# Optimization experiments

Measured on AMD Instinct MI355X. Metric: run time of the kernel, lower is better.

Reference implementation:

```python
import jax, jax.numpy as jnp
import numpy as np

D_MODEL = 1024
B, T = 4, 2048
LN_EPS = 1e-5


def setup_inputs() -> dict:
    key = jax.random.key(0)
    ks = jax.random.split(key, 8)
    d = D_MODEL
    x = jax.random.normal(ks[0], (B, T, d), dtype=jnp.float32)
    # linear params (fan-in scaled)
    W_in = jax.random.normal(ks[1], (d, 4 * d), dtype=jnp.float32) / np.sqrt(d)
    b_in = jnp.zeros((4 * d,), dtype=jnp.float32)
    W_out = jax.random.normal(ks[2], (2 * d, d), dtype=jnp.float32) / np.sqrt(2 * d)
    b_out = jnp.zeros((d,), dtype=jnp.float32)
    # LRU initializer (matches the torch module's initializer())
    rng = np.random.default_rng(0)
    r_min, r_max = 0.9, 0.999
    u1 = rng.random(d)
    u2 = rng.random(d)
    nu_log = np.log(-0.5 * np.log(u1 * (r_max ** 2 - r_min ** 2) + r_min ** 2))
    theta_log = np.log(u2 * np.pi * 2)
    gamma_log = np.log(np.sqrt(1 - np.exp(-np.exp(nu_log)) ** 2))
    # LayerNorm affine params
    ln_w = jnp.ones((2 * d,), dtype=jnp.float32)
    ln_b = jnp.zeros((2 * d,), dtype=jnp.float32)
    return {
        "x": x,
        "W_in": W_in, "b_in": b_in,
        "nu_log": jnp.asarray(nu_log, dtype=jnp.float32),
        "theta_log": jnp.asarray(theta_log, dtype=jnp.float32),
        "gamma_log": jnp.asarray(gamma_log, dtype=jnp.float32),
        "ln_w": ln_w, "ln_b": ln_b,
        "W_out": W_out, "b_out": b_out,
    }


def _complex_scan(in_r, in_i, f_r, f_i):
    """h_t = f * h_{t-1} + in_t over axis=1, complex math in real/imag pairs."""
    def combine(l, r):
        a1r, a1i, b1r, b1i = l
        a2r, a2i, b2r, b2i = r
        ar = a2r * a1r - a2i * a1i
        ai = a2r * a1i + a2i * a1r
        br = a2r * b1r - a2i * b1i + b2r
        bi = a2r * b1i + a2i * b1r + b2i
        return (ar, ai, br, bi)
    fr = jnp.broadcast_to(f_r, in_r.shape)
    fi = jnp.broadcast_to(f_i, in_i.shape)
    _, _, hr, hi = jax.lax.associative_scan(combine, (fr, fi, in_r, in_i), axis=1)
    return hr, hi


def reference(x, W_in, b_in, nu_log, theta_log, gamma_log, ln_w, ln_b, W_out, b_out):
    d = x.shape[-1]
    u = x @ W_in + b_in                       # [B, T, 4d]
    v, o = u[..., :2 * d], u[..., 2 * d:]     # each [B, T, 2d]
    nu = jnp.exp(-jnp.exp(nu_log))            # [d]
    theta = jnp.exp(theta_log)
    gamma = jnpp_exp = jnp.exp(gamma_log)
    f_r = nu * jnp.cos(theta)
    f_i = nu * jnp.sin(theta)
    in_r = gamma * v[..., :d]                 # [B, T, d]
    in_i = gamma * v[..., d:]
    h_r, h_i = _complex_scan(in_r, in_i, f_r, f_i)
    y = jnp.concatenate([h_r, h_i], axis=-1) * jax.nn.silu(o)  # [B, T, 2d]
    mu = jnp.mean(y, axis=-1, keepdims=True)
    var = jnp.mean(jnp.square(y - mu), axis=-1, keepdims=True)
    y = (y - mu) * jax.lax.rsqrt(var + LN_EPS) * ln_w + ln_b
    return y @ W_out + b_out                  # [B, T, d]
```

## Files before the change

kernel.cpp:

```cpp
#include <hip/hip_runtime.h>
#include <hip/hip_bf16.h>

#define D_MODEL 1024
#define BB 4
#define TT 2048
#define ROWS (BB*TT)
#define NCHUNK 64
#define CHLEN 32

typedef __attribute__((ext_vector_type(8))) short short8;
typedef __attribute__((ext_vector_type(4))) float floatx4;

static __device__ __forceinline__ ushort f2bf(float f) {
    union { float f; unsigned u; } v; v.f = f;
    unsigned r = v.u + 0x7FFF + ((v.u >> 16) & 1);
    return (ushort)(r >> 16);
}
static __device__ __forceinline__ float bf2f(ushort b) {
    union { unsigned u; float f; } v; v.u = ((unsigned)b) << 16;
    return v.f;
}

#define GLOAD_LDS16(gp, lp)                                                 \
    __builtin_amdgcn_global_load_lds(                                       \
        (const __attribute__((address_space(1))) void*)(gp),                \
        (__attribute__((address_space(3))) void*)(lp), 16, 0, 0)

#define PREP_A 8192
#define PREP_B 4096
#define PREP_C 2048
__global__ __launch_bounds__(256) void prep_all(
    const float* __restrict__ x, ushort* __restrict__ xb,
    const float* __restrict__ W_in, ushort* __restrict__ WinT,
    const float* __restrict__ W_out, ushort* __restrict__ W1T,
    const float* __restrict__ lnw, const float* __restrict__ lnb,
    float* __restrict__ s1, float* __restrict__ c2,
    const float* __restrict__ nu_log, const float* __restrict__ theta_log,
    const float* __restrict__ gamma_log,
    float* __restrict__ fr, float* __restrict__ fi, float* __restrict__ gm) {
    __shared__ float smem[32 * 33 + 8 * 32 * 2];
    int bid = blockIdx.x, tid = threadIdx.x;
    if (bid < PREP_A) {
        int i = bid * 256 + tid;
        float4 v = ((const float4*)x)[i];
        ushort4 o;
        o.x = f2bf(v.x); o.y = f2bf(v.y); o.z = f2bf(v.z); o.w = f2bf(v.w);
        ((ushort4*)xb)[i] = o;
    } else if (bid < PREP_A + PREP_B) {
        int b2 = bid - PREP_A;
        int n0 = (b2 & 127) * 32, k0 = (b2 >> 7) * 32;
        int tx = tid & 31, ty = tid >> 5;
        float (*tile)[33] = (float (*)[33])smem;
#pragma unroll
        for (int j = 0; j < 4; ++j)
            tile[ty + j*8][tx] = W_in[(size_t)(k0 + ty + j*8) * 4096 + n0 + tx];
        __syncthreads();
#pragma unroll
        for (int j = 0; j < 4; ++j)
            WinT[(size_t)(n0 + ty + j*8) * 1024 + k0 + tx] = f2bf(tile[tx][ty + j*8]);
    } else if (bid < PREP_A + PREP_B + PREP_C) {
        int b2 = bid - PREP_A - PREP_B;
        int n0 = (b2 & 31) * 32, k0 = (b2 >> 5) * 32;
        int tx = tid & 31, ty = tid >> 5;
        float (*tile)[33] = (float (*)[33])smem;
        float* red1 = smem + 32 * 33;
        float* red2 = red1 + 8 * 32;
        float p1 = 0.f, p2 = 0.f;
#pragma unroll
        for (int j = 0; j < 4; ++j) {
            int k = k0 + ty + j * 8;
            float w = W_out[(size_t)k * 1024 + n0 + tx];
            float lw = lnw[k], lb = lnb[k];
            tile[ty + j*8][tx] = lw * w;
            p1 += lw * w; p2 += lb * w;
        }
        __syncthreads();
#pragma unroll
        for (int j = 0; j < 4; ++j)
            W1T[(size_t)(n0 + ty + j*8) * 2048 + k0 + tx] = f2bf(tile[tx][ty + j*8]);
        red1[ty * 32 + tx] = p1; red2[ty * 32 + tx] = p2;
        __syncthreads();
        if (ty == 0) {
            float a = 0.f, b = 0.f;
#pragma unroll
            for (int t = 0; t < 8; ++t) { a += red1[t * 32 + tx]; b += red2[t * 32 + tx]; }
            atomicAdd(&s1[n0 + tx], a);
            atomicAdd(&c2[n0 + tx], b);
        }
    } else {
        int c = (bid - PREP_A - PREP_B - PREP_C) * 256 + tid;
        if (c < D_MODEL) {
            float nu = expf(-expf(nu_log[c]));
            float th = expf(theta_log[c]);
            fr[c] = nu * cosf(th);
            fi[c] = nu * sinf(th);
            gm[c] = expf(gamma_log[c]);
        }
    }
}

#define P_PRE  do { __builtin_amdgcn_sched_barrier(0); __builtin_amdgcn_s_barrier();  \
                    asm volatile("s_waitcnt lgkmcnt(0)" ::: "memory");                \
                    __builtin_amdgcn_sched_barrier(0);                                \
                    __builtin_amdgcn_s_setprio(1); } while (0)
#define P_POST do { __builtin_amdgcn_s_setprio(0); __builtin_amdgcn_sched_barrier(0); \
                    __builtin_amdgcn_s_barrier();                                     \
                    __builtin_amdgcn_sched_barrier(0); } while (0)

__global__ __launch_bounds__(512) void gemm256(
    const ushort* __restrict__ A, const ushort* __restrict__ B,
    int K, const float* __restrict__ bias,
    const float* __restrict__ gamma,
    ushort* __restrict__ out_r, ushort* __restrict__ out_i,
    ushort* __restrict__ out_o) {
    __shared__ ushort LA[2][256 * 64];
    __shared__ ushort LB[2][256 * 64];
    int tid = threadIdx.x;
    int lane = tid & 63;
    int wave = tid >> 6;
    int wp = wave >> 2;
    int wq = wave & 3;
    int lr = lane & 15, q = lane >> 4;
    int swl = lr & 7;
    int rs8 = tid >> 3, ch = tid & 7;
    int sw8 = (ch ^ (rs8 & 7)) * 8;

    int gx = gridDim.x;
    int nwg = gx * gridDim.y;
    int lid = blockIdx.y * gx + blockIdx.x;
    int per = nwg >> 3;
    int sid = (lid & 7) * per + (lid >> 3);
    long m0 = (long)(sid / gx) * 256;
    long n0 = (long)(sid % gx) * 256;
    const int NT = K >> 6;

    const ushort* Abase = A + (size_t)(m0 + rs8) * K + sw8;
    const ushort* Bbase = B + (size_t)(n0 + rs8) * K + sw8;

    floatx4 acc[8][4] = {};

#define STG_A(kt, P, R) GLOAD_LDS16(Abase + (size_t)(R) * K + (kt), \
                                    &LA[P][((R) + rs8) * 64 + ch * 8])
#define STG_B(kt, P, R) GLOAD_LDS16(Bbase + (size_t)(R) * K + (kt), \
                                    &LB[P][((R) + rs8) * 64 + ch * 8])

    STG_A(0, 0, 0);    STG_A(0, 0, 64);
    STG_B(0, 0, 0);    STG_B(0, 0, 64);
    STG_B(0, 0, 128);  STG_B(0, 0, 192);
    STG_A(0, 0, 128);  STG_A(0, 0, 192);
    STG_A(64, 1, 0);   STG_A(64, 1, 64);
    STG_B(64, 1, 0);   STG_B(64, 1, 64);
    STG_B(64, 1, 128); STG_B(64, 1, 192);
    asm volatile("s_waitcnt vmcnt(6)" ::: "memory");
    __builtin_amdgcn_s_barrier();

    for (int t = 0; t < NT; ++t) {
        const int p = t & 1;
        int kt1 = (t + 1 < NT) ? (t + 1) << 6 : 0;
        int kt2 = (t + 2 < NT) ? (t + 2) << 6 : 0;
        short8 a[2][4], b0[2][2], b1[2][2];

#pragma unroll
        for (int ks = 0; ks < 2; ++ks) {
#pragma unroll
            for (int r = 0; r < 4; ++r)
                a[ks][r] = *(const short8*)&LA[p][(wp * 64 + r * 16 + lr) * 64 + ((ks * 4 + q) ^ swl) * 8];
#pragma unroll
            for (int c = 0; c < 2; ++c)
                b0[ks][c] = *(const short8*)&LB[p][(wq * 32 + c * 16 + lr) * 64 + ((ks * 4 + q) ^ swl) * 8];
        }
        STG_A(kt1, p ^ 1, 128); STG_A(kt1, p ^ 1, 192);
        P_PRE;
#pragma unroll
        for (int ks = 0; ks < 2; ++ks)
#pragma unroll
            for (int r = 0; r < 4; ++r)
#pragma unroll
                for (int c = 0; c < 2; ++c)
                    acc[r][c] = __builtin_amdgcn_mfma_f32_16x16x32_bf16(
                        a[ks][r], b0[ks][c], acc[r][c], 0, 0, 0);
        P_POST;

#pragma unroll
        for (int ks = 0; ks < 2; ++ks)
#pragma unroll
            for (int c = 0; c < 2; ++c)
                b1[ks][c] = *(const short8*)&LB[p][(128 + wq * 32 + c * 16 + lr) * 64 + ((ks * 4 + q) ^ swl) * 8];
        STG_A(kt2, p, 0); STG_A(kt2, p, 64);
        P_PRE;
#pragma unroll
        for (int ks = 0; ks < 2; ++ks)
#pragma unroll
            for (int r = 0; r < 4; ++r)
#pragma unroll
                for (int c = 0; c < 2; ++c)
                    acc[r][2 + c] = __builtin_amdgcn_mfma_f32_16x16x32_bf16(
                        a[ks][r], b1[ks][c], acc[r][2 + c], 0, 0, 0);
        P_POST;

#pragma unroll
        for (int ks = 0; ks < 2; ++ks)
#pragma unroll
            for (int r = 0; r < 4; ++r)
                a[ks][r] = *(const short8*)&LA[p][(128 + wp * 64 + r * 16 + lr) * 64 + ((ks * 4 + q) ^ swl) * 8];
        STG_B(kt2, p, 0); STG_B(kt2, p, 64);
        P_PRE;
#pragma unroll
        for (int ks = 0; ks < 2; ++ks)
#pragma unroll
            for (int r = 0; r < 4; ++r)
#pragma unroll
                for (int c = 0; c < 2; ++c)
                    acc[4 + r][c] = __builtin_amdgcn_mfma_f32_16x16x32_bf16(
                        a[ks][r], b0[ks][c], acc[4 + r][c], 0, 0, 0);
        P_POST;

        STG_B(kt2, p, 128); STG_B(kt2, p, 192);
        asm volatile("s_waitcnt vmcnt(6)" ::: "memory");
        P_PRE;
#pragma unroll
        for (int ks = 0; ks < 2; ++ks)
#pragma unroll
            for (int r = 0; r < 4; ++r)
#pragma unroll
                for (int c = 0; c < 2; ++c)
                    acc[4 + r][2 + c] = __builtin_amdgcn_mfma_f32_16x16x32_bf16(
                        a[ks][r], b1[ks][c], acc[4 + r][2 + c], 0, 0, 0);
        P_POST;
    }
    asm volatile("s_waitcnt vmcnt(0)" ::: "memory");

    int sector = (int)(n0 >> 10);
    if (sector < 2) {
        ushort* dst = sector ? out_i : out_r;
#pragma unroll
        for (int nh = 0; nh < 2; ++nh)
#pragma unroll
            for (int c = 0; c < 2; ++c) {
                int lc = (int)(n0 & 1023) + nh * 128 + wq * 32 + c * 16 + lr;
                float bv = bias[(sector << 10) + lc];
                float gv = gamma[lc];
#pragma unroll
                for (int mh = 0; mh < 2; ++mh)
#pragma unroll
                    for (int r = 0; r < 4; ++r)
#pragma unroll
                        for (int g = 0; g < 4; ++g) {
                            long row = m0 + mh * 128 + wp * 64 + r * 16 + q * 4 + g;
                            dst[row * 1024 + lc] = f2bf(gv * (acc[mh * 4 + r][nh * 2 + c][g] + bv));
                        }
            }
    } else {
        int oc0 = (int)(n0 - 2048);
#pragma unroll
        for (int nh = 0; nh < 2; ++nh)
#pragma unroll
            for (int c = 0; c < 2; ++c) {
                int oc = oc0 + nh * 128 + wq * 32 + c * 16 + lr;
                float bv = bias[2048 + oc];
#pragma unroll
                for (int mh = 0; mh < 2; ++mh)
#pragma unroll
                    for (int r = 0; r < 4; ++r)
#pragma unroll
                        for (int g = 0; g < 4; ++g) {
                            long row = m0 + mh * 128 + wp * 64 + r * 16 + q * 4 + g;
                            out_o[row * 2048 + oc] = f2bf(acc[mh * 4 + r][nh * 2 + c][g] + bv);
                        }
            }
    }
#undef STG_A
#undef STG_B
}

__global__ __launch_bounds__(512) void gemm2_2t(
    const ushort* __restrict__ A, const ushort* __restrict__ B,
    int K, int N, const float* __restrict__ bias, float* __restrict__ outC,
    const float* __restrict__ mu, const float* __restrict__ rs,
    const float* __restrict__ s1, const float* __restrict__ c2) {
    __shared__ ushort LA[2][128 * 64];
    __shared__ ushort LB[2][256 * 64];
    int tid = threadIdx.x;
    int lane = tid & 63;
    int wave = tid >> 6;
    int wp = wave >> 2;
    int wq = wave & 3;
    int lr = lane & 15, q = lane >> 4;
    int swl = lr & 7;
    int rs8 = tid >> 3, ch = tid & 7;
    int sw8 = (ch ^ (rs8 & 7)) * 8;

    int gx = gridDim.x;
    int nwg = gx * gridDim.y;
    int lid = blockIdx.y * gx + blockIdx.x;
    int per = nwg >> 3;
    int sid = (lid & 7) * per + (lid >> 3);
    long m0 = (long)(sid / gx) * 128;
    long n0 = (long)(sid % gx) * 256;
    const int NT = K >> 6;
    const int NI = NT >> 1;

    const ushort* Abase = A + (size_t)(m0 + rs8) * K + sw8;
    const ushort* Bbase = B + (size_t)(n0 + rs8) * K + sw8;

    floatx4 acc[4][4] = {};

#define STG2_A(kt, P, R) GLOAD_LDS16(Abase + (size_t)(R) * K + (kt), \
                                     &LA[P][((R) + rs8) * 64 + ch * 8])
#define STG2_B(kt, P, R) GLOAD_LDS16(Bbase + (size_t)(R) * K + (kt), \
                                     &LB[P][((R) + rs8) * 64 + ch * 8])
#define STG2_TILE(kt, P) do { STG2_A(kt, P, 0); STG2_A(kt, P, 64);            \
                              STG2_B(kt, P, 0); STG2_B(kt, P, 64);            \
                              STG2_B(kt, P, 128); STG2_B(kt, P, 192); } while (0)

    STG2_TILE(0, 0);
    asm volatile("s_waitcnt vmcnt(0)" ::: "memory");
    __builtin_amdgcn_s_barrier();

    for (int i = 0; i < NI; ++i) {
        int t0 = 2 * i;
        int kt1 = (t0 + 1) << 6;
        int kt2 = (t0 + 2 < NT) ? (t0 + 2) << 6 : 0;
        short8 a[2][2], b0[2][2], b1[2][2];

#pragma unroll
        for (int ks = 0; ks < 2; ++ks) {
#pragma unroll
            for (int r = 0; r < 2; ++r)
                a[ks][r] = *(const short8*)&LA[0][(wp * 32 + r * 16 + lr) * 64 + ((ks * 4 + q) ^ swl) * 8];
#pragma unroll
            for (int c = 0; c < 2; ++c) {
                b0[ks][c] = *(const short8*)&LB[0][(wq * 32 + c * 16 + lr) * 64 + ((ks * 4 + q) ^ swl) * 8];
                b1[ks][c] = *(const short8*)&LB[0][(128 + wq * 32 + c * 16 + lr) * 64 + ((ks * 4 + q) ^ swl) * 8];
            }
        }
        STG2_TILE(kt1, 1);
        P_PRE;
#pragma unroll
        for (int ks = 0; ks < 2; ++ks)
#pragma unroll
            for (int r = 0; r < 2; ++r)
#pragma unroll
                for (int c = 0; c < 2; ++c) {
                    acc[r][c] = __builtin_amdgcn_mfma_f32_16x16x32_bf16(
                        a[ks][r], b0[ks][c], acc[r][c], 0, 0, 0);
                    acc[r][2 + c] = __builtin_amdgcn_mfma_f32_16x16x32_bf16(
                        a[ks][r], b1[ks][c], acc[r][2 + c], 0, 0, 0);
                }
        P_POST;

#pragma unroll
        for (int ks = 0; ks < 2; ++ks)
#pragma unroll
            for (int r = 0; r < 2; ++r)
                a[ks][r] = *(const short8*)&LA[0][(64 + wp * 32 + r * 16 + lr) * 64 + ((ks * 4 + q) ^ swl) * 8];
        P_PRE;
#pragma unroll
        for (int ks = 0; ks < 2; ++ks)
#pragma unroll
            for (int r = 0; r < 2; ++r)
#pragma unroll
                for (int c = 0; c < 2; ++c) {
                    acc[2 + r][c] = __builtin_amdgcn_mfma_f32_16x16x32_bf16(
                        a[ks][r], b0[ks][c], acc[2 + r][c], 0, 0, 0);
                    acc[2 + r][2 + c] = __builtin_amdgcn_mfma_f32_16x16x32_bf16(
                        a[ks][r], b1[ks][c], acc[2 + r][2 + c], 0, 0, 0);
                }
        asm volatile("s_waitcnt vmcnt(0)" ::: "memory");
        P_POST;

#pragma unroll
        for (int ks = 0; ks < 2; ++ks) {
#pragma unroll
            for (int r = 0; r < 2; ++r)
                a[ks][r] = *(const short8*)&LA[1][(wp * 32 + r * 16 + lr) * 64 + ((ks * 4 + q) ^ swl) * 8];
#pragma unroll
            for (int c = 0; c < 2; ++c) {
                b0[ks][c] = *(const short8*)&LB[1][(wq * 32 + c * 16 + lr) * 64 + ((ks * 4 + q) ^ swl) * 8];
                b1[ks][c] = *(const short8*)&LB[1][(128 + wq * 32 + c * 16 + lr) * 64 + ((ks * 4 + q) ^ swl) * 8];
            }
        }
        STG2_TILE(kt2, 0);
        P_PRE;
#pragma unroll
        for (int ks = 0; ks < 2; ++ks)
#pragma unroll
            for (int r = 0; r < 2; ++r)
#pragma unroll
                for (int c = 0; c < 2; ++c) {
                    acc[r][c] = __builtin_amdgcn_mfma_f32_16x16x32_bf16(
                        a[ks][r], b0[ks][c], acc[r][c], 0, 0, 0);
                    acc[r][2 + c] = __builtin_amdgcn_mfma_f32_16x16x32_bf16(
                        a[ks][r], b1[ks][c], acc[r][2 + c], 0, 0, 0);
                }
        P_POST;

#pragma unroll
        for (int ks = 0; ks < 2; ++ks)
#pragma unroll
            for (int r = 0; r < 2; ++r)
                a[ks][r] = *(const short8*)&LA[1][(64 + wp * 32 + r * 16 + lr) * 64 + ((ks * 4 + q) ^ swl) * 8];
        P_PRE;
#pragma unroll
        for (int ks = 0; ks < 2; ++ks)
#pragma unroll
            for (int r = 0; r < 2; ++r)
#pragma unroll
                for (int c = 0; c < 2; ++c) {
                    acc[2 + r][c] = __builtin_amdgcn_mfma_f32_16x16x32_bf16(
                        a[ks][r], b0[ks][c], acc[2 + r][c], 0, 0, 0);
                    acc[2 + r][2 + c] = __builtin_amdgcn_mfma_f32_16x16x32_bf16(
                        a[ks][r], b1[ks][c], acc[2 + r][2 + c], 0, 0, 0);
                }
        asm volatile("s_waitcnt vmcnt(0)" ::: "memory");
        P_POST;
    }
    asm volatile("s_waitcnt vmcnt(0)" ::: "memory");

#pragma unroll
    for (int nh = 0; nh < 2; ++nh)
#pragma unroll
        for (int c = 0; c < 2; ++c) {
            long col = n0 + nh * 128 + wq * 32 + c * 16 + lr;
            float bc = c2[col] + bias[col];
            float s1c = s1[col];
#pragma unroll
            for (int mh = 0; mh < 2; ++mh)
#pragma unroll
                for (int r = 0; r < 2; ++r)
#pragma unroll
                    for (int g = 0; g < 4; ++g) {
                        long row = m0 + mh * 64 + wp * 32 + r * 16 + q * 4 + g;
                        outC[row * (long)N + col] =
                            rs[row] * (acc[mh * 2 + r][nh * 2 + c][g] - mu[row] * s1c) + bc;
                    }
        }
#undef STG2_A
#undef STG2_B
#undef STG2_TILE
}

__global__ __launch_bounds__(256) void scan_carries(
    const ushort* __restrict__ in_r, const ushort* __restrict__ in_i,
    float* __restrict__ carry,
    const float* __restrict__ fr_, const float* __restrict__ fi_) {
    int t = blockIdx.x * 256 + threadIdx.x;
    int cp = t & 511;
    int ck = (t >> 9) & (NCHUNK - 1);
    int b = t >> 15;
    int c0 = cp * 2;
    float f0r = fr_[c0], f0i = fi_[c0], f1r = fr_[c0 + 1], f1i = fi_[c0 + 1];
    size_t base = ((size_t)(b * TT + ck * CHLEN)) * 1024 + c0;
    float h0r = 0.f, h0i = 0.f, h1r = 0.f, h1i = 0.f;
#pragma unroll 8
    for (int j = 0; j < CHLEN; ++j) {
        uint ur = *(const uint*)(in_r + base + (size_t)j * 1024);
        uint ui = *(const uint*)(in_i + base + (size_t)j * 1024);
        float r0 = bf2f((ushort)ur), r1 = bf2f((ushort)(ur >> 16));
        float i0 = bf2f((ushort)ui), i1 = bf2f((ushort)(ui >> 16));
        float n0r = f0r * h0r - f0i * h0i + r0;
        float n0i = f0r * h0i + f0i * h0r + i0;
        float n1r = f1r * h1r - f1i * h1i + r1;
        float n1i = f1r * h1i + f1i * h1r + i1;
        h0r = n0r; h0i = n0i; h1r = n1r; h1i = n1i;
    }
    ((float4*)carry)[((size_t)b * NCHUNK + ck) * 512 + cp] =
        make_float4(h0r, h0i, h1r, h1i);
}

__global__ __launch_bounds__(256) void carry_prefix(
    float* __restrict__ carry,
    const float* __restrict__ fr_, const float* __restrict__ fi_) {
    int t = blockIdx.x * 256 + threadIdx.x;
    int cp = t & 511, b = t >> 9;
    int c0 = cp * 2;
    float a0r = fr_[c0], a0i = fi_[c0], a1r = fr_[c0 + 1], a1i = fi_[c0 + 1];
#pragma unroll
    for (int s = 0; s < 5; ++s) {
        float t0r = a0r * a0r - a0i * a0i, t0i = 2.f * a0r * a0i;
        float t1r = a1r * a1r - a1i * a1i, t1i = 2.f * a1r * a1i;
        a0r = t0r; a0i = t0i; a1r = t1r; a1i = t1i;
    }
    float4* base = (float4*)carry + (size_t)b * NCHUNK * 512 + cp;
    float C0r = 0.f, C0i = 0.f, C1r = 0.f, C1i = 0.f;
    for (int k = 0; k < NCHUNK; ++k) {
        float4 s = base[(size_t)k * 512];
        base[(size_t)k * 512] = make_float4(C0r, C0i, C1r, C1i);
        float n0r = a0r * C0r - a0i * C0i + s.x;
        float n0i = a0r * C0i + a0i * C0r + s.y;
        float n1r = a1r * C1r - a1i * C1i + s.z;
        float n1i = a1r * C1i + a1i * C1r + s.w;
        C0r = n0r; C0i = n0i; C1r = n1r; C1i = n1i;
    }
}

__global__ __launch_bounds__(256) void scan_apply(
    const ushort* __restrict__ in_r, const ushort* __restrict__ in_i,
    const float* __restrict__ carry,
    const float* __restrict__ fr_, const float* __restrict__ fi_,
    const ushort* __restrict__ o, ushort* __restrict__ yb) {
    int t = blockIdx.x * 256 + threadIdx.x;
    int cp = t & 511;
    int ck = (t >> 9) & (NCHUNK - 1);
    int b = t >> 15;
    int c0 = cp * 2;
    float f0r = fr_[c0], f0i = fi_[c0], f1r = fr_[c0 + 1], f1i = fi_[c0 + 1];
    float4 C = ((const float4*)carry)[((size_t)b * NCHUNK + ck) * 512 + cp];
    float h0r = C.x, h0i = C.y, h1r = C.z, h1i = C.w;
    size_t base = ((size_t)(b * TT + ck * CHLEN)) * 1024 + c0;
    size_t rowbase = (size_t)(b * TT + ck * CHLEN);
#pragma unroll 4
    for (int j = 0; j < CHLEN; ++j) {
        uint ur = *(const uint*)(in_r + base + (size_t)j * 1024);
        uint ui = *(const uint*)(in_i + base + (size_t)j * 1024);
        size_t ob = (rowbase + j) * 2048 + c0;
        uint uo1 = *(const uint*)(o + ob);
        uint uo2 = *(const uint*)(o + ob + 1024);
        float r0 = bf2f((ushort)ur), r1 = bf2f((ushort)(ur >> 16));
        float i0 = bf2f((ushort)ui), i1 = bf2f((ushort)(ui >> 16));
        float n0r = f0r * h0r - f0i * h0i + r0;
        float n0i = f0r * h0i + f0i * h0r + i0;
        float n1r = f1r * h1r - f1i * h1i + r1;
        float n1i = f1r * h1i + f1i * h1r + i1;
        h0r = n0r; h0i = n0i; h1r = n1r; h1i = n1i;
        float o00 = bf2f((ushort)uo1), o01 = bf2f((ushort)(uo1 >> 16));
        float o10 = bf2f((ushort)uo2), o11 = bf2f((ushort)(uo2 >> 16));
        float y00 = h0r * o00 / (1.f + __expf(-o00));
        float y01 = h1r * o01 / (1.f + __expf(-o01));
        float y10 = h0i * o10 / (1.f + __expf(-o10));
        float y11 = h1i * o11 / (1.f + __expf(-o11));
        *(uint*)(yb + ob) = (uint)f2bf(y00) | ((uint)f2bf(y01) << 16);
        *(uint*)(yb + ob + 1024) = (uint)f2bf(y10) | ((uint)f2bf(y11) << 16);
    }
}

__global__ __launch_bounds__(256) void row_stats(
    const ushort* __restrict__ yb, float* __restrict__ mu_o,
    float* __restrict__ rs_o) {
    long row = blockIdx.x;
    int tid = threadIdx.x;
    const ushort* p = yb + row * 2048 + tid * 8;
    uint4 raw = *(const uint4*)p;
    float s = 0.f, s2 = 0.f;
    unsigned w[4] = {raw.x, raw.y, raw.z, raw.w};
#pragma unroll
    for (int j = 0; j < 4; ++j) {
        float a = bf2f((ushort)(w[j] & 0xffff));
        float b = bf2f((ushort)(w[j] >> 16));
        s += a + b; s2 += a * a + b * b;
    }
#pragma unroll
    for (int off = 32; off > 0; off >>= 1) {
        s += __shfl_down(s, off, 64);
        s2 += __shfl_down(s2, off, 64);
    }
    __shared__ float red[8];
    int wv = tid >> 6;
    if ((tid & 63) == 0) { red[wv] = s; red[4 + wv] = s2; }
    __syncthreads();
    if (tid == 0) {
        s = red[0] + red[1] + red[2] + red[3];
        s2 = red[4] + red[5] + red[6] + red[7];
        float mu = s * (1.f / 2048.f);
        float var = s2 * (1.f / 2048.f) - mu * mu;
        mu_o[row] = mu;
        rs_o[row] = rsqrtf(var + 1e-5f);
    }
}


extern "C" void kernel_launch(void* const* d_in, const int* in_sizes, int n_in,
                              void* d_out, int out_size, void* d_ws, size_t ws_size,
                              hipStream_t stream) {
    const float* x         = (const float*)d_in[0];
    const float* W_in      = (const float*)d_in[1];
    const float* b_in      = (const float*)d_in[2];
    const float* nu_log    = (const float*)d_in[3];
    const float* theta_log = (const float*)d_in[4];
    const float* gamma_log = (const float*)d_in[5];
    const float* ln_w      = (const float*)d_in[6];
    const float* ln_b      = (const float*)d_in[7];
    const float* W_out     = (const float*)d_in[8];
    const float* b_out     = (const float*)d_in[9];
    float* out = (float*)d_out;

    char* ws = (char*)d_ws;
    size_t off = 0;
    auto alloc = [&](size_t bytes) {
        char* p = ws + off;
        off += (bytes + 255) & ~(size_t)255;
        return p;
    };
    ushort* xb    = (ushort*)alloc((size_t)ROWS * 1024 * 2);
    ushort* WinT  = (ushort*)alloc((size_t)4096 * 1024 * 2);
    ushort* W1T   = (ushort*)alloc((size_t)1024 * 2048 * 2);
    float*  fr    = (float*)alloc(1024 * 4);
    float*  fi    = (float*)alloc(1024 * 4);
    float*  gm    = (float*)alloc(1024 * 4);
    float*  s1c2  = (float*)alloc(2048 * 4);
    float*  s1    = s1c2;
    float*  c2    = s1c2 + 1024;
    ushort* in_r  = (ushort*)alloc((size_t)ROWS * 1024 * 2);
    ushort* in_i  = (ushort*)alloc((size_t)ROWS * 1024 * 2);
    ushort* obuf  = (ushort*)alloc((size_t)ROWS * 2048 * 2);
    float*  carry = (float*)alloc((size_t)BB * 1024 * NCHUNK * 2 * 4);
    ushort* yb    = (ushort*)alloc((size_t)ROWS * 2048 * 2);
    float*  muv   = (float*)alloc(ROWS * 4);
    float*  rsv   = (float*)alloc(ROWS * 4);

    hipMemsetAsync(s1c2, 0, 2048 * 4, stream);

    prep_all<<<PREP_A + PREP_B + PREP_C + 4, 256, 0, stream>>>(
        x, xb, W_in, WinT, W_out, W1T, ln_w, ln_b, s1, c2,
        nu_log, theta_log, gamma_log, fr, fi, gm);

    gemm256<<<dim3(4096 / 256, ROWS / 256), 512, 0, stream>>>(
        xb, WinT, 1024, b_in, gm, in_r, in_i, obuf);

    scan_carries<<<BB * 512 * NCHUNK / 256, 256, 0, stream>>>(in_r, in_i, carry, fr, fi);
    carry_prefix<<<BB * 512 / 256, 256, 0, stream>>>(carry, fr, fi);
    scan_apply<<<BB * 512 * NCHUNK / 256, 256, 0, stream>>>(
        in_r, in_i, carry, fr, fi, obuf, yb);

    row_stats<<<ROWS, 256, 0, stream>>>(yb, muv, rsv);

    gemm2_2t<<<dim3(1024 / 256, ROWS / 128), 512, 0, stream>>>(
        yb, W1T, 2048, 1024, b_out, out, muv, rsv, s1, c2);
}
```

Baseline: 276.4 us.

## Fuse LayerNorm row stats into GEMM2 and carry prefix into scan_apply

```diff
diff --git a/kernel.cpp b/kernel.cpp
--- a/kernel.cpp
+++ b/kernel.cpp
@@ -276,10 +276,10 @@
 __global__ __launch_bounds__(512) void gemm2_2t(
     const ushort* __restrict__ A, const ushort* __restrict__ B,
     int K, int N, const float* __restrict__ bias, float* __restrict__ outC,
-    const float* __restrict__ mu, const float* __restrict__ rs,
     const float* __restrict__ s1, const float* __restrict__ c2) {
     __shared__ ushort LA[2][128 * 64];
     __shared__ ushort LB[2][256 * 64];
+    __shared__ float mu_s[128], rs_s[128];
     int tid = threadIdx.x;
     int lane = tid & 63;
     int wave = tid >> 6;
@@ -289,6 +289,7 @@
     int swl = lr & 7;
     int rs8 = tid >> 3, ch = tid & 7;
     int sw8 = (ch ^ (rs8 & 7)) * 8;
+    int srow = tid >> 2, sj4 = tid & 3;
 
     int gx = gridDim.x;
     int nwg = gx * gridDim.y;
@@ -304,6 +305,7 @@
     const ushort* Bbase = B + (size_t)(n0 + rs8) * K + sw8;
 
     floatx4 acc[4][4] = {};
+    float st1 = 0.f, st2 = 0.f;
 
 #define STG2_A(kt, P, R) GLOAD_LDS16(Abase + (size_t)(R) * K + (kt), \
                                      &LA[P][((R) + rs8) * 64 + ch * 8])
@@ -312,6 +314,12 @@
 #define STG2_TILE(kt, P) do { STG2_A(kt, P, 0); STG2_A(kt, P, 64);            \
                               STG2_B(kt, P, 0); STG2_B(kt, P, 64);            \
                               STG2_B(kt, P, 128); STG2_B(kt, P, 192); } while (0)
+#define STAT_ACC(sv) do {                                                     \
+        _Pragma("unroll")                                                     \
+        for (int e = 0; e < 8; ++e) {                                         \
+            float v_ = bf2f((ushort)(sv)[e]);                                 \
+            st1 += v_; st2 += v_ * v_;                                        \
+        } } while (0)
 
     STG2_TILE(0, 0);
     asm volatile("s_waitcnt vmcnt(0)" ::: "memory");
@@ -321,7 +329,7 @@
         int t0 = 2 * i;
         int kt1 = (t0 + 1) << 6;
         int kt2 = (t0 + 2 < NT) ? (t0 + 2) << 6 : 0;
-        short8 a[2][2], b0[2][2], b1[2][2];
+        short8 a[2][2], b0[2][2], b1[2][2], sv0, sv1;
 
 #pragma unroll
         for (int ks = 0; ks < 2; ++ks) {
@@ -334,6 +342,8 @@
                 b1[ks][c] = *(const short8*)&LB[0][(128 + wq * 32 + c * 16 + lr) * 64 + ((ks * 4 + q) ^ swl) * 8];
             }
         }
+        sv0 = *(const short8*)&LA[0][srow * 64 + sj4 * 16];
+        sv1 = *(const short8*)&LA[0][srow * 64 + sj4 * 16 + 8];
         STG2_TILE(kt1, 1);
         P_PRE;
 #pragma unroll
@@ -347,6 +357,7 @@
                     acc[r][2 + c] = __builtin_amdgcn_mfma_f32_16x16x32_bf16(
                         a[ks][r], b1[ks][c], acc[r][2 + c], 0, 0, 0);
                 }
+        STAT_ACC(sv0); STAT_ACC(sv1);
         P_POST;
 
 #pragma unroll
@@ -380,6 +391,8 @@
                 b1[ks][c] = *(const short8*)&LB[1][(128 + wq * 32 + c * 16 + lr) * 64 + ((ks * 4 + q) ^ swl) * 8];
             }
         }
+        sv0 = *(const short8*)&LA[1][srow * 64 + sj4 * 16];
+        sv1 = *(const short8*)&LA[1][srow * 64 + sj4 * 16 + 8];
         STG2_TILE(kt2, 0);
         P_PRE;
 #pragma unroll
@@ -393,6 +406,7 @@
                     acc[r][2 + c] = __builtin_amdgcn_mfma_f32_16x16x32_bf16(
                         a[ks][r], b1[ks][c], acc[r][2 + c], 0, 0, 0);
                 }
+        STAT_ACC(sv0); STAT_ACC(sv1);
         P_POST;
 
 #pragma unroll
@@ -417,6 +431,16 @@
     }
     asm volatile("s_waitcnt vmcnt(0)" ::: "memory");
 
+    st1 += __shfl_down(st1, 1, 64); st1 += __shfl_down(st1, 2, 64);
+    st2 += __shfl_down(st2, 1, 64); st2 += __shfl_down(st2, 2, 64);
+    if ((tid & 3) == 0) {
+        float mu = st1 * (1.f / 2048.f);
+        float var = st2 * (1.f / 2048.f) - mu * mu;
+        mu_s[srow] = mu;
+        rs_s[srow] = rsqrtf(var + 1e-5f);
+    }
+    __syncthreads();
+
 #pragma unroll
     for (int nh = 0; nh < 2; ++nh)
 #pragma unroll
@@ -430,14 +454,16 @@
                 for (int r = 0; r < 2; ++r)
 #pragma unroll
                     for (int g = 0; g < 4; ++g) {
-                        long row = m0 + mh * 64 + wp * 32 + r * 16 + q * 4 + g;
-                        outC[row * (long)N + col] =
-                            rs[row] * (acc[mh * 2 + r][nh * 2 + c][g] - mu[row] * s1c) + bc;
+                        int lrow = mh * 64 + wp * 32 + r * 16 + q * 4 + g;
+                        outC[(m0 + lrow) * (long)N + col] =
+                            rs_s[lrow] * (acc[mh * 2 + r][nh * 2 + c][g]
+                                          - mu_s[lrow] * s1c) + bc;
                     }
         }
 #undef STG2_A
 #undef STG2_B
 #undef STG2_TILE
+#undef STAT_ACC
 }
 
 __global__ __launch_bounds__(256) void scan_carries(
@@ -468,32 +494,6 @@
         make_float4(h0r, h0i, h1r, h1i);
 }
 
-__global__ __launch_bounds__(256) void carry_prefix(
-    float* __restrict__ carry,
-    const float* __restrict__ fr_, const float* __restrict__ fi_) {
-    int t = blockIdx.x * 256 + threadIdx.x;
-    int cp = t & 511, b = t >> 9;
-    int c0 = cp * 2;
-    float a0r = fr_[c0], a0i = fi_[c0], a1r = fr_[c0 + 1], a1i = fi_[c0 + 1];
-#pragma unroll
-    for (int s = 0; s < 5; ++s) {
-        float t0r = a0r * a0r - a0i * a0i, t0i = 2.f * a0r * a0i;
-        float t1r = a1r * a1r - a1i * a1i, t1i = 2.f * a1r * a1i;
-        a0r = t0r; a0i = t0i; a1r = t1r; a1i = t1i;
-    }
-    float4* base = (float4*)carry + (size_t)b * NCHUNK * 512 + cp;
-    float C0r = 0.f, C0i = 0.f, C1r = 0.f, C1i = 0.f;
-    for (int k = 0; k < NCHUNK; ++k) {
-        float4 s = base[(size_t)k * 512];
-        base[(size_t)k * 512] = make_float4(C0r, C0i, C1r, C1i);
-        float n0r = a0r * C0r - a0i * C0i + s.x;
-        float n0i = a0r * C0i + a0i * C0r + s.y;
-        float n1r = a1r * C1r - a1i * C1i + s.z;
-        float n1i = a1r * C1i + a1i * C1r + s.w;
-        C0r = n0r; C0i = n0i; C1r = n1r; C1i = n1i;
-    }
-}
-
 __global__ __launch_bounds__(256) void scan_apply(
     const ushort* __restrict__ in_r, const ushort* __restrict__ in_i,
     const float* __restrict__ carry,
@@ -505,8 +505,25 @@
     int b = t >> 15;
     int c0 = cp * 2;
     float f0r = fr_[c0], f0i = fi_[c0], f1r = fr_[c0 + 1], f1i = fi_[c0 + 1];
-    float4 C = ((const float4*)carry)[((size_t)b * NCHUNK + ck) * 512 + cp];
-    float h0r = C.x, h0i = C.y, h1r = C.z, h1i = C.w;
+
+    float a0r = f0r, a0i = f0i, a1r = f1r, a1i = f1i;
+#pragma unroll
+    for (int s = 0; s < 5; ++s) {
+        float t0r = a0r * a0r - a0i * a0i, t0i = 2.f * a0r * a0i;
+        float t1r = a1r * a1r - a1i * a1i, t1i = 2.f * a1r * a1i;
+        a0r = t0r; a0i = t0i; a1r = t1r; a1i = t1i;
+    }
+    const float4* cb = (const float4*)carry + (size_t)b * NCHUNK * 512 + cp;
+    float h0r = 0.f, h0i = 0.f, h1r = 0.f, h1i = 0.f;
+    for (int k = 0; k < ck; ++k) {
+        float4 s = cb[(size_t)k * 512];
+        float n0r = a0r * h0r - a0i * h0i + s.x;
+        float n0i = a0r * h0i + a0i * h0r + s.y;
+        float n1r = a1r * h1r - a1i * h1i + s.z;
+        float n1i = a1r * h1i + a1i * h1r + s.w;
+        h0r = n0r; h0i = n0i; h1r = n1r; h1i = n1i;
+    }
+
     size_t base = ((size_t)(b * TT + ck * CHLEN)) * 1024 + c0;
     size_t rowbase = (size_t)(b * TT + ck * CHLEN);
 #pragma unroll 4
@@ -534,40 +551,6 @@
     }
 }
 
-__global__ __launch_bounds__(256) void row_stats(
-    const ushort* __restrict__ yb, float* __restrict__ mu_o,
-    float* __restrict__ rs_o) {
-    long row = blockIdx.x;
-    int tid = threadIdx.x;
-    const ushort* p = yb + row * 2048 + tid * 8;
-    uint4 raw = *(const uint4*)p;
-    float s = 0.f, s2 = 0.f;
-    unsigned w[4] = {raw.x, raw.y, raw.z, raw.w};
-#pragma unroll
-    for (int j = 0; j < 4; ++j) {
-        float a = bf2f((ushort)(w[j] & 0xffff));
-        float b = bf2f((ushort)(w[j] >> 16));
-        s += a + b; s2 += a * a + b * b;
-    }
-#pragma unroll
-    for (int off = 32; off > 0; off >>= 1) {
-        s += __shfl_down(s, off, 64);
-        s2 += __shfl_down(s2, off, 64);
-    }
-    __shared__ float red[8];
-    int wv = tid >> 6;
-    if ((tid & 63) == 0) { red[wv] = s; red[4 + wv] = s2; }
-    __syncthreads();
-    if (tid == 0) {
-        s = red[0] + red[1] + red[2] + red[3];
-        s2 = red[4] + red[5] + red[6] + red[7];
-        float mu = s * (1.f / 2048.f);
-        float var = s2 * (1.f / 2048.f) - mu * mu;
-        mu_o[row] = mu;
-        rs_o[row] = rsqrtf(var + 1e-5f);
-    }
-}
-
 
 extern "C" void kernel_launch(void* const* d_in, const int* in_sizes, int n_in,
                               void* d_out, int out_size, void* d_ws, size_t ws_size,
@@ -603,10 +586,8 @@
     ushort* in_r  = (ushort*)alloc((size_t)ROWS * 1024 * 2);
     ushort* in_i  = (ushort*)alloc((size_t)ROWS * 1024 * 2);
     ushort* obuf  = (ushort*)alloc((size_t)ROWS * 2048 * 2);
-    float*  carry = (float*)alloc((size_t)BB * 1024 * NCHUNK * 2 * 4);
+    float*  carry = (float*)alloc((size_t)BB * 512 * NCHUNK * 4 * 4);
     ushort* yb    = (ushort*)alloc((size_t)ROWS * 2048 * 2);
-    float*  muv   = (float*)alloc(ROWS * 4);
-    float*  rsv   = (float*)alloc(ROWS * 4);
 
     hipMemsetAsync(s1c2, 0, 2048 * 4, stream);
 
@@ -618,12 +599,10 @@
         xb, WinT, 1024, b_in, gm, in_r, in_i, obuf);
 
     scan_carries<<<BB * 512 * NCHUNK / 256, 256, 0, stream>>>(in_r, in_i, carry, fr, fi);
-    carry_prefix<<<BB * 512 / 256, 256, 0, stream>>>(carry, fr, fi);
+
     scan_apply<<<BB * 512 * NCHUNK / 256, 256, 0, stream>>>(
         in_r, in_i, carry, fr, fi, obuf, yb);
 
-    row_stats<<<ROWS, 256, 0, stream>>>(yb, muv, rsv);
-
     gemm2_2t<<<dim3(1024 / 256, ROWS / 128), 512, 0, stream>>>(
-        yb, W1T, 2048, 1024, b_out, out, muv, rsv, s1, c2);
-}
+        yb, W1T, 2048, 1024, b_out, out, s1, c2);
+}
```

Result: slower. 284.5 us (median of 2 runs) (+2.9%).
